# Kernel optimization log

Hardware: AMD Instinct MI355X
Metric: run time of the kernel (lower is better)

Reference implementation:

```python
import jax, jax.numpy as jnp
import numpy as np

EPS = 1e-5

def _layer_norm(x, w, b):
    mu = jnp.mean(x, axis=-1, keepdims=True)
    var = jnp.mean(jnp.square(x - mu), axis=-1, keepdims=True)
    return (x - mu) * jax.lax.rsqrt(var + EPS) * w + b

def setup_inputs() -> dict:
    key = jax.random.key(0)
    ks = jax.random.split(key, 8)
    B, S, D = 8, 2048, 1024
    image_features = jax.random.normal(ks[0], (B, S, D), dtype=jnp.float32)
    text_features = jax.random.normal(ks[1], (B, S, D), dtype=jnp.float32)
    ln_w = jnp.ones((D,), dtype=jnp.float32)
    ln_b = jnp.zeros((D,), dtype=jnp.float32)
    lim = 1.0 / np.sqrt(D)
    W_img = jax.random.uniform(ks[2], (D, D), minval=-lim, maxval=lim, dtype=jnp.float32)
    b_img = jax.random.uniform(ks[3], (D,), minval=-lim, maxval=lim, dtype=jnp.float32)
    W_txt = jax.random.uniform(ks[4], (D, D), minval=-lim, maxval=lim, dtype=jnp.float32)
    b_txt = jax.random.uniform(ks[5], (D,), minval=-lim, maxval=lim, dtype=jnp.float32)
    return {"image_features": image_features, "text_features": text_features,
            "ln_w": ln_w, "ln_b": ln_b, "W_img": W_img, "b_img": b_img,
            "W_txt": W_txt, "b_txt": b_txt}

def reference(image_features, text_features, ln_w, ln_b, W_img, b_img, W_txt, b_txt):
    D = image_features.shape[-1]
    scale = D ** (-0.5)
    image_norm = _layer_norm(image_features, ln_w, ln_b)
    text_norm = _layer_norm(text_features, ln_w, ln_b)
    # torch Linear: x @ W^T + b
    image_proj = jnp.einsum('bsd,ed->bse', image_norm, W_img) + b_img  # [B,Si,D]
    text_proj = jnp.einsum('btd,ed->bte', text_norm, W_txt) + b_txt    # [B,St,D]
    attn = jnp.einsum('bsd,btd->bst', image_proj, text_proj) * scale   # [B,Si,St]
    attn = jax.nn.softmax(attn, axis=-1)
    image_out = jnp.einsum('bst,btd->bsd', attn, text_proj)            # [B,Si,D]
    text_out = jnp.einsum('bst,bsd->btd', attn, image_proj)            # [B,St,D]
    return (image_out, text_out)
```

## Files before the change

### kernel.cpp

```cpp
#include <hip/hip_runtime.h>


#define DEV __device__ __forceinline__

typedef short s16x8 __attribute__((ext_vector_type(8)));
typedef float f32x4 __attribute__((ext_vector_type(4)));

DEV unsigned short f2bf(float f){
  unsigned u = __float_as_uint(f);
  u = (u + 0x7fffu + ((u >> 16) & 1u)) >> 16;
  return (unsigned short)u;
}
DEV float bf2f(unsigned short s){ return __uint_as_float(((unsigned)s) << 16); }

DEV void ldsload16(const void* g, void* l){
  __builtin_amdgcn_global_load_lds((const __attribute__((address_space(1))) void*)g,
                                   (__attribute__((address_space(3))) void*)l, 16, 0, 0);
}

__global__ __launch_bounds__(256) void k_cvt(const float* __restrict__ src,
                                             unsigned short* __restrict__ dst, int n4){
  int i = blockIdx.x * 256 + threadIdx.x;
  if (i < n4){
    float4 v = ((const float4*)src)[i];
    ushort4 o;
    o.x = f2bf(v.x); o.y = f2bf(v.y); o.z = f2bf(v.z); o.w = f2bf(v.w);
    ((ushort4*)dst)[i] = o;
  }
}

__global__ __launch_bounds__(256) void k_ln(const float* __restrict__ x,
                                            const float* __restrict__ w,
                                            const float* __restrict__ b,
                                            unsigned short* __restrict__ y){
  int row = blockIdx.x, tid = threadIdx.x;
  float4 v = ((const float4*)(x + (size_t)row * 1024))[tid];
  float s  = v.x + v.y + v.z + v.w;
  float s2 = v.x*v.x + v.y*v.y + v.z*v.z + v.w*v.w;
  #pragma unroll
  for (int o = 32; o > 0; o >>= 1){ s += __shfl_xor(s, o, 64); s2 += __shfl_xor(s2, o, 64); }
  __shared__ float sh[8];
  int wv = tid >> 6, ln = tid & 63;
  if (!ln){ sh[wv] = s; sh[4 + wv] = s2; }
  __syncthreads();
  s  = sh[0] + sh[1] + sh[2] + sh[3];
  s2 = sh[4] + sh[5] + sh[6] + sh[7];
  float mean = s * (1.f/1024.f);
  float var  = s2 * (1.f/1024.f) - mean * mean;
  float rstd = rsqrtf(var + 1e-5f);
  float4 w4 = ((const float4*)w)[tid];
  float4 b4 = ((const float4*)b)[tid];
  ushort4 o;
  o.x = f2bf((v.x-mean)*rstd*w4.x + b4.x);
  o.y = f2bf((v.y-mean)*rstd*w4.y + b4.y);
  o.z = f2bf((v.z-mean)*rstd*w4.z + b4.z);
  o.w = f2bf((v.w-mean)*rstd*w4.w + b4.w);
  ((ushort4*)(y + (size_t)row * 1024))[tid] = o;
}

#define STG(MAT, BASE, LD, T) do{                                                 \
  ldsload16((BASE) + (size_t)(wave*16 + sfr) * (LD) + (T)*32 + sq*8,              \
            &MAT[(T)&1][wave][0]);                                                \
  ldsload16((BASE) + (size_t)(wave*16 + 64 + sfr) * (LD) + (T)*32 + sq*8,         \
            &MAT[(T)&1][wave + 4][0]);                                            \
}while(0)

template<int OUT_BF16>
__global__ __launch_bounds__(256, 3) void k_gemm128(const unsigned short* __restrict__ A,
                                                    const unsigned short* __restrict__ Bt,
                                                    void* __restrict__ C,
                                                    const float* __restrict__ bias, float scale,
                                                    int K, int lda, int ldb, int ldc,
                                                    long sA, long sB, long sC,
                                                    int NBX, int NBY){
  __shared__ __align__(16) unsigned short As[2][8][512];
  __shared__ __align__(16) unsigned short Bs[2][8][512];
  int nwg = gridDim.x;
  int bid = blockIdx.x;
  int swz = (bid & 7) * (nwg >> 3) + (bid >> 3);
  int bx = swz % NBX; int rem = swz / NBX;
  int by = rem % NBY; int bz = rem / NBY;

  int tid = threadIdx.x, lane = tid & 63, wave = tid >> 6;
  int wm = wave >> 1, wn = wave & 1;
  int q = lane >> 4, fr = lane & 15;
  const unsigned short* Ab = A  + (size_t)bz * sA + (size_t)by * 128 * lda;
  const unsigned short* Bb = Bt + (size_t)bz * sB + (size_t)bx * 128 * ldb;
  int v   = (lane & 7) ^ ((lane >> 3) & 7);
  int sfr = 2 * (lane >> 3) + (v >> 2);
  int sq  = v & 3;
  int roff = ((fr >> 1) << 6) + (((q + ((fr & 1) << 2)) ^ ((fr >> 1) & 7)) << 3);
  const int NT = K >> 5;

  f32x4 acc[4][4];
  #pragma unroll
  for (int m = 0; m < 4; ++m)
    #pragma unroll
    for (int n = 0; n < 4; ++n) acc[m][n] = f32x4{0.f, 0.f, 0.f, 0.f};

  STG(As, Ab, lda, 0); STG(Bs, Bb, ldb, 0);
  asm volatile("s_waitcnt vmcnt(0)");
  __builtin_amdgcn_s_barrier();

  for (int t = 0; t < NT; ++t){
    const int buf = t & 1;
    if (t + 1 < NT){ STG(As, Ab, lda, t + 1); STG(Bs, Bb, ldb, t + 1); }
    s16x8 af[4], bfr[4];
    #pragma unroll
    for (int mi = 0; mi < 4; ++mi) af[mi] = *(const s16x8*)&As[buf][wm*4 + mi][roff];
    #pragma unroll
    for (int n = 0; n < 4; ++n)   bfr[n]  = *(const s16x8*)&Bs[buf][wn*4 + n][roff];
    asm volatile("s_waitcnt lgkmcnt(0)");
    __builtin_amdgcn_sched_barrier(0);
    __builtin_amdgcn_s_setprio(1);
    #pragma unroll
    for (int mi = 0; mi < 4; ++mi)
      #pragma unroll
      for (int n = 0; n < 4; ++n)
        acc[mi][n] = __builtin_amdgcn_mfma_f32_16x16x32_bf16(af[mi], bfr[n], acc[mi][n], 0, 0, 0);
    __builtin_amdgcn_s_setprio(0);
    __builtin_amdgcn_sched_barrier(0);
    asm volatile("s_waitcnt vmcnt(0)");
    __builtin_amdgcn_s_barrier();
  }
  size_t cb = (size_t)bz * sC;
  int row0 = by*128 + wm*64 + q*4;
  int col0 = bx*128 + wn*64 + fr;
  #pragma unroll
  for (int m = 0; m < 4; ++m){
    #pragma unroll
    for (int n = 0; n < 4; ++n){
      int col = col0 + n*16;
      float bv = bias ? bias[col] : 0.f;
      #pragma unroll
      for (int j = 0; j < 4; ++j){
        int row = row0 + m*16 + j;
        float vv = acc[m][n][j] * scale + bv;
        if (OUT_BF16) ((unsigned short*)C)[cb + (size_t)row*ldc + col] = f2bf(vv);
        else          ((float*)C)[cb + (size_t)row*ldc + col] = vv;
      }
    }
  }
}

__global__ __launch_bounds__(256) void k_transpose(const unsigned short* __restrict__ src,
                                                   unsigned short* __restrict__ dst,
                                                   int R, int C, long sS, long sD){
  __shared__ __align__(16) unsigned short tile[64 * 64];
  int tid = threadIdx.x;
  const unsigned short* sb = src + (size_t)blockIdx.z * sS;
  unsigned short* db = dst + (size_t)blockIdx.z * sD;
  int r0 = blockIdx.y * 64, c0 = blockIdx.x * 64;
  #pragma unroll
  for (int i = 0; i < 2; ++i){
    int ci = i * 256 + tid;
    int row = ci >> 3, cch = ci & 7;
    int pos = cch ^ (row & 7) ^ (row >> 3);
    uint4 v = *(const uint4*)&sb[(size_t)(r0 + row) * C + c0 + cch * 8];
    *(uint4*)&tile[row * 64 + pos * 8] = v;
  }
  __syncthreads();
  int ocp = tid >> 3, og = tid & 7;
  int oc = ocp * 2;
  union { uint4 v; unsigned short us[8]; } o0, o1;
  #pragma unroll
  for (int k = 0; k < 8; ++k){
    int r = og * 8 + k;
    int pos = (oc >> 3) ^ (r & 7) ^ (r >> 3);
    unsigned pr = *(const unsigned*)&tile[r * 64 + pos * 8 + (oc & 7)];
    o0.us[k] = (unsigned short)(pr & 0xffffu);
    o1.us[k] = (unsigned short)(pr >> 16);
  }
  *(uint4*)&db[(size_t)(c0 + oc    ) * R + r0 + og * 8] = o0.v;
  *(uint4*)&db[(size_t)(c0 + oc + 1) * R + r0 + og * 8] = o1.v;
}

__global__ __launch_bounds__(256) void k_softmax_t(unsigned short* __restrict__ a,
                                                   unsigned short* __restrict__ at){
  __shared__ __align__(16) unsigned short tile[64 * 64];
  int tid = threadIdx.x;
  int r = tid >> 2, sub = tid & 3;
  size_t boff = (size_t)blockIdx.y * 4194304;
  int r0 = blockIdx.x * 64;
  unsigned short* prow = a + boff + (size_t)(r0 + r) * 2048;
  float mx = -3.0e38f;
  for (int i = 0; i < 64; ++i){
    union { uint4 v; unsigned short us[8]; } u;
    u.v = *(const uint4*)&prow[(sub + 4*i) * 8];
    #pragma unroll
    for (int j = 0; j < 8; ++j) mx = fmaxf(mx, bf2f(u.us[j]));
  }
  mx = fmaxf(mx, __shfl_xor(mx, 1, 64));
  mx = fmaxf(mx, __shfl_xor(mx, 2, 64));
  float s = 0.f;
  for (int i = 0; i < 64; ++i){
    union { uint4 v; unsigned short us[8]; } u;
    u.v = *(const uint4*)&prow[(sub + 4*i) * 8];
    #pragma unroll
    for (int j = 0; j < 8; ++j) s += __expf(bf2f(u.us[j]) - mx);
  }
  s += __shfl_xor(s, 1, 64);
  s += __shfl_xor(s, 2, 64);
  float inv = 1.f / s;
  int ocp = tid >> 3, og = tid & 7, oc = ocp * 2;
  for (int cb = 0; cb < 32; ++cb){
    #pragma unroll
    for (int jj = 0; jj < 2; ++jj){
      int j = sub + jj*4;
      int c8 = cb*8 + j;
      union { uint4 v; unsigned short us[8]; } u, o;
      u.v = *(const uint4*)&prow[c8 * 8];
      #pragma unroll
      for (int k = 0; k < 8; ++k) o.us[k] = f2bf(__expf(bf2f(u.us[k]) - mx) * inv);
      *(uint4*)&prow[c8 * 8] = o.v;
      int pos = j ^ (r & 7) ^ (r >> 3);
      *(uint4*)&tile[r * 64 + pos * 8] = o.v;
    }
    __syncthreads();
    union { uint4 v; unsigned short us[8]; } o0, o1;
    #pragma unroll
    for (int k = 0; k < 8; ++k){
      int rr = og * 8 + k;
      int pos = (oc >> 3) ^ (rr & 7) ^ (rr >> 3);
      unsigned pr = *(const unsigned*)&tile[rr * 64 + pos * 8 + (oc & 7)];
      o0.us[k] = (unsigned short)(pr & 0xffffu);
      o1.us[k] = (unsigned short)(pr >> 16);
    }
    size_t c0 = (size_t)cb * 64;
    *(uint4*)&at[boff + (c0 + oc    ) * 2048 + r0 + og * 8] = o0.v;
    *(uint4*)&at[boff + (c0 + oc + 1) * 2048 + r0 + og * 8] = o1.v;
    __syncthreads();
  }
}

extern "C" void kernel_launch(void* const* d_in, const int* in_sizes, int n_in,
                              void* d_out, int out_size, void* d_ws, size_t ws_size,
                              hipStream_t stream) {
  const float* img  = (const float*)d_in[0];
  const float* txt  = (const float*)d_in[1];
  const float* lnw  = (const float*)d_in[2];
  const float* lnb  = (const float*)d_in[3];
  const float* Wimg = (const float*)d_in[4];
  const float* bimg = (const float*)d_in[5];
  const float* Wtxt = (const float*)d_in[6];
  const float* btxt = (const float*)d_in[7];
  float* out = (float*)d_out;

  char* ws = (char*)d_ws;
  unsigned short* R1 = (unsigned short*)ws;
  unsigned short* R2 = (unsigned short*)(ws + 67108864);
  unsigned short* WB = (unsigned short*)(ws + 134217728);
  unsigned short* R4 = (unsigned short*)(ws + 138412032);

  const long PB = 2097152;
  const long AB = 4194304;

  k_cvt<<<1024, 256, 0, stream>>>(Wimg, WB,           262144);
  k_cvt<<<1024, 256, 0, stream>>>(Wtxt, WB + 1048576, 262144);
  k_ln<<<16384, 256, 0, stream>>>(img, lnw, lnb, R1);
  k_ln<<<16384, 256, 0, stream>>>(txt, lnw, lnb, R1 + 16777216);
  k_gemm128<1><<<1024, 256, 0, stream>>>(R1,            WB,           R2,            bimg, 1.f,
                                         1024, 1024, 1024, 1024, 0, 0, 0, 8, 128);
  k_gemm128<1><<<1024, 256, 0, stream>>>(R1 + 16777216, WB + 1048576, R2 + 16777216, btxt, 1.f,
                                         1024, 1024, 1024, 1024, 0, 0, 0, 8, 128);
  dim3 gt(16, 32, 8);
  k_transpose<<<gt, 256, 0, stream>>>(R2,            R1,            2048, 1024, PB, PB);
  k_transpose<<<gt, 256, 0, stream>>>(R2 + 16777216, R1 + 16777216, 2048, 1024, PB, PB);
  k_gemm128<1><<<2048, 256, 0, stream>>>(R2, R2 + 16777216, R4, nullptr, 0.03125f,
                                         1024, 1024, 1024, 2048, PB, PB, AB, 16, 16);
  dim3 gs(32, 8);
  k_softmax_t<<<gs, 256, 0, stream>>>(R4, R2);
  k_gemm128<0><<<1024, 256, 0, stream>>>(R4, R1 + 16777216, out, nullptr, 1.f,
                                         2048, 2048, 2048, 1024, AB, PB, PB, 8, 16);
  k_gemm128<0><<<1024, 256, 0, stream>>>(R2, R1, out + 16777216, nullptr, 1.f,
                                         2048, 2048, 2048, 1024, AB, PB, PB, 8, 16);
}
```

Measured before the change: 457.5 us.

## Triple-buffer GEMM LDS staging, online softmax, and merge weight conversions

The GEMM moves from double to triple LDS buffering with two tiles prefetched ahead, and waits on partial vmcnt so loads stay in flight across iterations. The softmax replaces its separate max pass and sum pass with a single online pass that rescales the running sum. The two weight-conversion launches become one. LDS use grows to 48KB per block, which may lower occupancy against launch_bounds(256,3), and the vmcnt counts must match the number of issued loads exactly.

Result: slower. 527.2 us (+15.2%).

```diff
diff --git a/kernel.cpp b/kernel.cpp
--- a/kernel.cpp
+++ b/kernel.cpp
@@ -18,15 +18,18 @@
                                    (__attribute__((address_space(3))) void*)l, 16, 0, 0);
 }
 
-__global__ __launch_bounds__(256) void k_cvt(const float* __restrict__ src,
-                                             unsigned short* __restrict__ dst, int n4){
+__global__ __launch_bounds__(256) void k_cvt2(const float* __restrict__ sa,
+                                              const float* __restrict__ sb,
+                                              unsigned short* __restrict__ da,
+                                              unsigned short* __restrict__ db, int n4){
   int i = blockIdx.x * 256 + threadIdx.x;
-  if (i < n4){
-    float4 v = ((const float4*)src)[i];
-    ushort4 o;
-    o.x = f2bf(v.x); o.y = f2bf(v.y); o.z = f2bf(v.z); o.w = f2bf(v.w);
-    ((ushort4*)dst)[i] = o;
-  }
+  const float* s; unsigned short* d; int j;
+  if (i < n4){ s = sa; d = da; j = i; }
+  else       { s = sb; d = db; j = i - n4; if (j >= n4) return; }
+  float4 v = ((const float4*)s)[j];
+  ushort4 o;
+  o.x = f2bf(v.x); o.y = f2bf(v.y); o.z = f2bf(v.z); o.w = f2bf(v.w);
+  ((ushort4*)d)[j] = o;
 }
 
 __global__ __launch_bounds__(256) void k_ln(const float* __restrict__ x,
@@ -58,11 +61,11 @@
   ((ushort4*)(y + (size_t)row * 1024))[tid] = o;
 }
 
-#define STG(MAT, BASE, LD, T) do{                                                 \
+#define STG(MAT, BASE, LD, T, SL) do{                                             \
   ldsload16((BASE) + (size_t)(wave*16 + sfr) * (LD) + (T)*32 + sq*8,              \
-            &MAT[(T)&1][wave][0]);                                                \
+            &MAT[SL][wave][0]);                                                   \
   ldsload16((BASE) + (size_t)(wave*16 + 64 + sfr) * (LD) + (T)*32 + sq*8,         \
-            &MAT[(T)&1][wave + 4][0]);                                            \
+            &MAT[SL][wave + 4][0]);                                               \
 }while(0)
 
 template<int OUT_BF16>
@@ -73,8 +76,8 @@
                                                     int K, int lda, int ldb, int ldc,
                                                     long sA, long sB, long sC,
                                                     int NBX, int NBY){
-  __shared__ __align__(16) unsigned short As[2][8][512];
-  __shared__ __align__(16) unsigned short Bs[2][8][512];
+  __shared__ __align__(16) unsigned short As[3][8][512];
+  __shared__ __align__(16) unsigned short Bs[3][8][512];
   int nwg = gridDim.x;
   int bid = blockIdx.x;
   int swz = (bid & 7) * (nwg >> 3) + (bid >> 3);
@@ -98,18 +101,20 @@
     #pragma unroll
     for (int n = 0; n < 4; ++n) acc[m][n] = f32x4{0.f, 0.f, 0.f, 0.f};
 
-  STG(As, Ab, lda, 0); STG(Bs, Bb, ldb, 0);
-  asm volatile("s_waitcnt vmcnt(0)");
+  STG(As, Ab, lda, 0, 0); STG(Bs, Bb, ldb, 0, 0);
+  STG(As, Ab, lda, 1, 1); STG(Bs, Bb, ldb, 1, 1);
+  STG(As, Ab, lda, 2, 2); STG(Bs, Bb, ldb, 2, 2);
+  asm volatile("s_waitcnt vmcnt(8)");
   __builtin_amdgcn_s_barrier();
 
+  int b0 = 0, ss = 2;
   for (int t = 0; t < NT; ++t){
-    const int buf = t & 1;
-    if (t + 1 < NT){ STG(As, Ab, lda, t + 1); STG(Bs, Bb, ldb, t + 1); }
+    if (t + 2 < NT){ STG(As, Ab, lda, t + 2, ss); STG(Bs, Bb, ldb, t + 2, ss); }
     s16x8 af[4], bfr[4];
     #pragma unroll
-    for (int mi = 0; mi < 4; ++mi) af[mi] = *(const s16x8*)&As[buf][wm*4 + mi][roff];
-    #pragma unroll
-    for (int n = 0; n < 4; ++n)   bfr[n]  = *(const s16x8*)&Bs[buf][wn*4 + n][roff];
+    for (int mi = 0; mi < 4; ++mi) af[mi] = *(const s16x8*)&As[b0][wm*4 + mi][roff];
+    #pragma unroll
+    for (int n = 0; n < 4; ++n)   bfr[n]  = *(const s16x8*)&Bs[b0][wn*4 + n][roff];
     asm volatile("s_waitcnt lgkmcnt(0)");
     __builtin_amdgcn_sched_barrier(0);
     __builtin_amdgcn_s_setprio(1);
@@ -120,8 +125,11 @@
         acc[mi][n] = __builtin_amdgcn_mfma_f32_16x16x32_bf16(af[mi], bfr[n], acc[mi][n], 0, 0, 0);
     __builtin_amdgcn_s_setprio(0);
     __builtin_amdgcn_sched_barrier(0);
-    asm volatile("s_waitcnt vmcnt(0)");
+    if (t + 2 < NT) asm volatile("s_waitcnt vmcnt(4)");
+    else            asm volatile("s_waitcnt vmcnt(0)");
     __builtin_amdgcn_s_barrier();
+    b0 = (b0 == 2) ? 0 : b0 + 1;
+    ss = (ss == 2) ? 0 : ss + 1;
   }
   size_t cb = (size_t)bz * sC;
   int row0 = by*128 + wm*64 + q*4;
@@ -183,24 +191,26 @@
   size_t boff = (size_t)blockIdx.y * 4194304;
   int r0 = blockIdx.x * 64;
   unsigned short* prow = a + boff + (size_t)(r0 + r) * 2048;
-  float mx = -3.0e38f;
+  float m = -3.0e38f, s = 0.f;
   for (int i = 0; i < 64; ++i){
     union { uint4 v; unsigned short us[8]; } u;
     u.v = *(const uint4*)&prow[(sub + 4*i) * 8];
-    #pragma unroll
-    for (int j = 0; j < 8; ++j) mx = fmaxf(mx, bf2f(u.us[j]));
-  }
-  mx = fmaxf(mx, __shfl_xor(mx, 1, 64));
-  mx = fmaxf(mx, __shfl_xor(mx, 2, 64));
-  float s = 0.f;
-  for (int i = 0; i < 64; ++i){
-    union { uint4 v; unsigned short us[8]; } u;
-    u.v = *(const uint4*)&prow[(sub + 4*i) * 8];
-    #pragma unroll
-    for (int j = 0; j < 8; ++j) s += __expf(bf2f(u.us[j]) - mx);
-  }
-  s += __shfl_xor(s, 1, 64);
-  s += __shfl_xor(s, 2, 64);
+    float x[8];
+    #pragma unroll
+    for (int j = 0; j < 8; ++j) x[j] = bf2f(u.us[j]);
+    float cm = fmaxf(fmaxf(fmaxf(x[0],x[1]),fmaxf(x[2],x[3])),
+                     fmaxf(fmaxf(x[4],x[5]),fmaxf(x[6],x[7])));
+    if (cm > m){ s *= __expf(m - cm); m = cm; }
+    #pragma unroll
+    for (int j = 0; j < 8; ++j) s += __expf(x[j] - m);
+  }
+  #pragma unroll
+  for (int o = 1; o <= 2; o <<= 1){
+    float mo = __shfl_xor(m, o, 64), so = __shfl_xor(s, o, 64);
+    float mn = fmaxf(m, mo);
+    s = s * __expf(m - mn) + so * __expf(mo - mn);
+    m = mn;
+  }
   float inv = 1.f / s;
   int ocp = tid >> 3, og = tid & 7, oc = ocp * 2;
   for (int cb = 0; cb < 32; ++cb){
@@ -211,7 +221,7 @@
       union { uint4 v; unsigned short us[8]; } u, o;
       u.v = *(const uint4*)&prow[c8 * 8];
       #pragma unroll
-      for (int k = 0; k < 8; ++k) o.us[k] = f2bf(__expf(bf2f(u.us[k]) - mx) * inv);
+      for (int k = 0; k < 8; ++k) o.us[k] = f2bf(__expf(bf2f(u.us[k]) - m) * inv);
       *(uint4*)&prow[c8 * 8] = o.v;
       int pos = j ^ (r & 7) ^ (r >> 3);
       *(uint4*)&tile[r * 64 + pos * 8] = o.v;
@@ -255,8 +265,7 @@
   const long PB = 2097152;
   const long AB = 4194304;
 
-  k_cvt<<<1024, 256, 0, stream>>>(Wimg, WB,           262144);
-  k_cvt<<<1024, 256, 0, stream>>>(Wtxt, WB + 1048576, 262144);
+  k_cvt2<<<2048, 256, 0, stream>>>(Wimg, Wtxt, WB, WB + 1048576, 262144);
   k_ln<<<16384, 256, 0, stream>>>(img, lnw, lnb, R1);
   k_ln<<<16384, 256, 0, stream>>>(txt, lnw, lnb, R1 + 16777216);
   k_gemm128<1><<<1024, 256, 0, stream>>>(R1,            WB,           R2,            bimg, 1.f,
```
